# Performance work log

Measured on AMD Instinct MI355X. Metric: run time of the kernel, lower is better.

## Reference

```python
import jax, jax.numpy as jnp
import numpy as np

H, P, G, NS, K = 8, 64, 64, 64, 3          # heads, dim_head, slice_num, d_state, d_conv
D_INNER = H * P                            # 512
CONV_DIM = D_INNER + 2 * NS                # 640
D_IN_PROJ = 2 * D_INNER + 2 * NS + 2 * H   # 1168


def setup_inputs() -> dict:
    key = jax.random.key(0)
    ks = jax.random.split(key, 10)
    dim, Bsz, N = 256, 4, 8192
    s = 0.02
    return {
        "x": jax.random.normal(ks[0], (Bsz, N, dim), jnp.float32),
        "W_fx": jax.random.normal(ks[1], (D_INNER, dim), jnp.float32) * s,
        "b_fx": jnp.zeros((D_INNER,), jnp.float32),
        "W_x": jax.random.normal(ks[2], (D_INNER, dim), jnp.float32) * s,
        "b_x": jnp.zeros((D_INNER,), jnp.float32),
        "W_slice": jax.random.normal(ks[3], (G, P), jnp.float32) * s,
        "b_slice": jnp.zeros((G,), jnp.float32),
        "temperature": jnp.full((1, H, 1, 1), 0.5, jnp.float32),
        "hy_in_w": jax.random.normal(ks[4], (D_IN_PROJ, D_INNER), jnp.float32) * s,
        "hy_conv_w": jax.random.normal(ks[5], (CONV_DIM, K), jnp.float32) * s,
        "hy_conv_b": jnp.zeros((CONV_DIM,), jnp.float32),
        "hy_dt_bias": jnp.log(jnp.expm1(jnp.full((H,), 0.01, jnp.float32))),
        "hy_A_log": jnp.log(jnp.linspace(1.0, 16.0, H)).astype(jnp.float32),
        "hy_D": jnp.ones((H,), jnp.float32),
        "hy_fcD_w": jax.random.normal(ks[6], (H, D_INNER), jnp.float32) * s,
        "hy_norm_w": jnp.ones((D_INNER,), jnp.float32),
        "hy_out_w": jax.random.normal(ks[7], (D_INNER, D_INNER), jnp.float32) * s,
        "out_w": jax.random.normal(ks[8], (dim, D_INNER), jnp.float32) * s,
        "out_b": jnp.zeros((dim,), jnp.float32),
    }


def _hydra(u, in_w, conv_w, conv_b, dt_bias, A_log, Dp, fcD_w, norm_w, out_w):
    # Bidirectional Mamba2-style selective scan (Hydra, non mem-eff path).
    Bt, L, _ = u.shape
    zxbcdt = u @ in_w.T                                   # (B, L, 1168)
    z = zxbcdt[..., :D_INNER]
    xBC = zxbcdt[..., D_INNER:D_INNER + CONV_DIM]
    dt = zxbcdt[..., -2 * H:]
    # fwd dts for fwd copies, time-flipped bwd dts stacked along batch
    dt = jnp.concatenate([dt[..., :H], jnp.flip(dt[..., H:], axis=1)], axis=0)
    dt = jax.nn.softplus(dt + dt_bias)                    # (2B, L, H)
    # depthwise causal conv, kernel K, left pad K-1 then silu
    xp = jnp.pad(xBC, ((0, 0), (K - 1, 0), (0, 0)))
    xBC = sum(xp[:, k:k + L, :] * conv_w[:, k] for k in range(K)) + conv_b
    xBC = jax.nn.silu(xBC)
    x = xBC[..., :D_INNER]
    Bm = xBC[..., D_INNER:D_INNER + NS]
    Cm = xBC[..., D_INNER + NS:]
    x_og = x
    x2 = jnp.concatenate([x, jnp.flip(x, 1)], 0).reshape(2 * Bt, L, H, P)
    B2 = jnp.concatenate([Bm, jnp.flip(Bm, 1)], 0)        # (2B, L, NS)
    C2 = jnp.concatenate([Cm, jnp.flip(Cm, 1)], 0)
    dA = jnp.exp(dt * (-jnp.exp(A_log)))                  # (2B, L, H)
    dBx = jnp.einsum('blh,bln,blhp->blhpn', dt, B2, x2)   # (2B, L, H, P, NS)

    def step(h, inp):
        dA_t, dBx_t, C_t = inp
        h = h * dA_t[:, :, None, None] + dBx_t
        return h, jnp.einsum('bhpn,bn->bhp', h, C_t)

    h0 = jnp.zeros((2 * Bt, H, P, NS), u.dtype)
    _, ys = jax.lax.scan(step, h0, (dA.transpose(1, 0, 2), dBx.transpose(1, 0, 2, 3, 4), C2.transpose(1, 0, 2)))
    y = ys.transpose(1, 0, 2, 3).reshape(2 * Bt, L, D_INNER)
    y_fw, y_bw = y[:Bt], jnp.flip(y[Bt:], 1)
    # quasiseparable: strictly-lower (shift fwd) + strictly-upper (shift bwd) + diagonal
    y = jnp.pad(y_fw[:, :-1], ((0, 0), (1, 0), (0, 0))) + jnp.pad(y_bw[:, 1:], ((0, 0), (0, 1), (0, 0)))
    y = y + x_og * jnp.repeat(x_og @ fcD_w.T + Dp, P, axis=-1)
    # gated RMSNorm (gate before norm), then out projection
    yg = y * jax.nn.silu(z)
    yg = yg * jax.lax.rsqrt(jnp.mean(jnp.square(yg), -1, keepdims=True) + 1e-5) * norm_w
    return yg @ out_w.T


def reference(x, W_fx, b_fx, W_x, b_x, W_slice, b_slice, temperature,
              hy_in_w, hy_conv_w, hy_conv_b, hy_dt_bias, hy_A_log, hy_D,
              hy_fcD_w, hy_norm_w, hy_out_w, out_w, out_b):
    B, N, _ = x.shape
    fx = (x @ W_fx.T + b_fx).reshape(B, N, H, P).transpose(0, 2, 1, 3)   # (B,H,N,P)
    xm = (x @ W_x.T + b_x).reshape(B, N, H, P).transpose(0, 2, 1, 3)
    temp = jnp.maximum(temperature, 1e-6)
    sw = jax.nn.softmax((xm @ W_slice.T + b_slice) / temp, axis=-1)      # (B,H,N,G)
    snorm = sw.sum(2)                                                     # (B,H,G)
    st = jnp.einsum('bhnc,bhng->bhgc', fx, sw) / (snorm + 1e-5)[..., None]
    st = st.transpose(0, 2, 1, 3).reshape(B, G, D_INNER)                  # (B,G,512)
    ot = _hydra(st, hy_in_w, hy_conv_w, hy_conv_b, hy_dt_bias, hy_A_log, hy_D,
                hy_fcD_w, hy_norm_w, hy_out_w)
    ot = ot.reshape(B, G, H, P).transpose(0, 2, 1, 3)                     # (B,H,G,P)
    out = jnp.einsum('bhgc,bhng->bhnc', ot, sw).transpose(0, 2, 1, 3).reshape(B, N, D_INNER)
    return out @ out_w.T + out_b
```

## Files before the change

kernel.cpp:

```cpp
#include <hip/hip_runtime.h>
#include <hip/hip_bf16.h>
#include <cstdint>
#include <cstddef>

#define Hh 8
#define DIN 512
#define CONVD 640
#define DPROJ 1168
#define NTOK 8192
#define DIM 256

typedef __attribute__((ext_vector_type(8))) short short8;
typedef __attribute__((ext_vector_type(4))) float f32x4;

static __device__ __forceinline__ float sigmoidf_(float x) { return 1.f / (1.f + expf(-x)); }
static __device__ __forceinline__ unsigned short f2b(float f) {
  __hip_bfloat16 h = __float2bfloat16(f);
  return *(unsigned short*)&h;
}
static __device__ __forceinline__ float b2f(unsigned short u) {
  union { unsigned int i; float f; } cv; cv.i = ((unsigned int)u) << 16; return cv.f;
}

__global__ __launch_bounds__(256) void k_cvt(
    const float* __restrict__ wfx, const float* __restrict__ wx, const float* __restrict__ outw,
    const float* __restrict__ inw, const float* __restrict__ how,
    const float* __restrict__ bfx, const float* __restrict__ bx,
    unsigned short* __restrict__ wcat, unsigned short* __restrict__ outwb,
    unsigned short* __restrict__ inwb, unsigned short* __restrict__ howb,
    float* __restrict__ bcat) {
  const int e = (blockIdx.x * 256 + threadIdx.x) * 4;
  if (e >= 1253376) {
    const int i = e - 1253376;
    float4 v;
    if (i < 512) v = *(const float4*)(bfx + i);
    else         v = *(const float4*)(bx + (i - 512));
    *(float4*)(bcat + i) = v;
    return;
  }
  const float* src; unsigned short* dst; int i;
  if (e < 131072)        { i = e;           src = wfx;  dst = wcat; }
  else if (e < 262144)   { i = e - 131072;  src = wx;   dst = wcat + 131072; }
  else if (e < 393216)   { i = e - 262144;  src = outw; dst = outwb; }
  else if (e < 991232)   { i = e - 393216;  src = inw;  dst = inwb; }
  else                   { i = e - 991232;  src = how;  dst = howb; }
  float4 v = *(const float4*)(src + i);
  ushort4 o;
  o.x = f2b(v.x); o.y = f2b(v.y); o.z = f2b(v.z); o.w = f2b(v.w);
  *(ushort4*)(dst + i) = o;
}

__global__ __launch_bounds__(256) void k_front(
    const float* __restrict__ x, const unsigned short* __restrict__ wcat,
    const float* __restrict__ bcat, const float* __restrict__ Wslice,
    const float* __restrict__ bslice, const float* __restrict__ temperature,
    unsigned short* __restrict__ cb, unsigned short* __restrict__ swb) {
  __shared__ unsigned short lds[17408];
  unsigned short* As = lds;
  unsigned short* Bs = lds + 8320;
  const int tid = threadIdx.x;
  const int m0 = blockIdx.x * 128;
  const int n0 = blockIdx.y * 128;
  const int w = tid >> 6, lane = tid & 63;
  const int l15 = lane & 15, kq = lane >> 4;
  const int wm = (w & 1) * 64, wn = (w >> 1) * 64;
  float bs[4];
#pragma unroll
  for (int j = 0; j < 4; ++j) bs[j] = bcat[n0 + wn + j * 16 + l15];
  f32x4 acc[4][4];
#pragma unroll
  for (int i = 0; i < 4; ++i)
#pragma unroll
    for (int j = 0; j < 4; ++j) acc[i][j] = (f32x4){0.f, 0.f, 0.f, 0.f};
  for (int kt = 0; kt < 256; kt += 64) {
#pragma unroll
    for (int i = 0; i < 4; ++i) {
      const int c = tid + 256 * i, m = c >> 3, kb = c & 7;
      const float* xs = &x[(size_t)(m0 + m) * 256 + kt + kb * 8];
      float4 v0 = *(const float4*)xs;
      float4 v1 = *(const float4*)(xs + 4);
      short8 av;
      av[0] = (short)f2b(v0.x); av[1] = (short)f2b(v0.y);
      av[2] = (short)f2b(v0.z); av[3] = (short)f2b(v0.w);
      av[4] = (short)f2b(v1.x); av[5] = (short)f2b(v1.y);
      av[6] = (short)f2b(v1.z); av[7] = (short)f2b(v1.w);
      *(short8*)&As[(kb * 130 + m) * 8] = av;
      *(short8*)&Bs[(kb * 130 + m) * 8] = *(const short8*)&wcat[(size_t)(n0 + m) * 256 + kt + kb * 8];
    }
    __syncthreads();
#pragma unroll
    for (int kw = 0; kw < 2; ++kw) {
      short8 af[4], bfr[4];
#pragma unroll
      for (int i = 0; i < 4; ++i) {
        af[i]  = *(const short8*)&As[((kw * 4 + kq) * 130 + wm + i * 16 + l15) * 8];
        bfr[i] = *(const short8*)&Bs[((kw * 4 + kq) * 130 + wn + i * 16 + l15) * 8];
      }
#pragma unroll
      for (int i = 0; i < 4; ++i)
#pragma unroll
        for (int j = 0; j < 4; ++j)
          acc[i][j] = __builtin_amdgcn_mfma_f32_16x16x32_bf16(af[i], bfr[j], acc[i][j], 0, 0, 0);
    }
    __syncthreads();
  }
  unsigned short* Cs = lds;
#pragma unroll
  for (int i = 0; i < 4; ++i)
#pragma unroll
    for (int j = 0; j < 4; ++j)
#pragma unroll
      for (int r = 0; r < 4; ++r) {
        const int m = wm + i * 16 + kq * 4 + r;
        const int n = wn + j * 16 + l15;
        Cs[m * 136 + n] = f2b(acc[i][j][r] + bs[j]);
      }
  __syncthreads();
  if (blockIdx.y < 4) {
#pragma unroll
    for (int it = 0; it < 8; ++it) {
      const int c = tid + 256 * it;
      const int m = c >> 4, seg = c & 15;
      *(short8*)&cb[(size_t)(m0 + m) * 512 + n0 + seg * 8] = *(const short8*)&Cs[m * 136 + seg * 8];
    }
    return;
  }
  const int h0 = (n0 - 512) >> 6;
  const int bidx = m0 >> 13, nb = m0 & (NTOK - 1);
  short8 sbfr[2][4];
#pragma unroll
  for (int kt = 0; kt < 2; ++kt)
#pragma unroll
    for (int j = 0; j < 4; ++j) {
      const float* wp = Wslice + (j * 16 + l15) * 64 + kt * 32 + kq * 8;
      short8 t;
#pragma unroll
      for (int u = 0; u < 8; ++u) t[u] = (short)f2b(wp[u]);
      sbfr[kt][j] = t;
    }
  float sbs[4];
#pragma unroll
  for (int j = 0; j < 4; ++j) sbs[j] = bslice[j * 16 + l15];
  f32x4 sacc[2][2][4];
#pragma unroll
  for (int hl = 0; hl < 2; ++hl)
#pragma unroll
    for (int i = 0; i < 2; ++i)
#pragma unroll
      for (int j = 0; j < 4; ++j) sacc[hl][i][j] = (f32x4){0.f, 0.f, 0.f, 0.f};
#pragma unroll
  for (int hl = 0; hl < 2; ++hl)
#pragma unroll
    for (int kt = 0; kt < 2; ++kt) {
      short8 af[2];
#pragma unroll
      for (int i = 0; i < 2; ++i)
        af[i] = *(const short8*)&Cs[(w * 32 + i * 16 + l15) * 136 + hl * 64 + kt * 32 + kq * 8];
#pragma unroll
      for (int i = 0; i < 2; ++i)
#pragma unroll
        for (int j = 0; j < 4; ++j)
          sacc[hl][i][j] = __builtin_amdgcn_mfma_f32_16x16x32_bf16(af[i], sbfr[kt][j], sacc[hl][i][j], 0, 0, 0);
    }
  __syncthreads();
#pragma unroll
  for (int hl = 0; hl < 2; ++hl) {
    const float invt = 1.f / fmaxf(temperature[h0 + hl], 1e-6f);
#pragma unroll
    for (int i = 0; i < 2; ++i)
#pragma unroll
      for (int r = 0; r < 4; ++r) {
        float v[4];
        float m = -1e30f;
#pragma unroll
        for (int j = 0; j < 4; ++j) { v[j] = (sacc[hl][i][j][r] + sbs[j]) * invt; m = fmaxf(m, v[j]); }
#pragma unroll
        for (int off = 8; off; off >>= 1) m = fmaxf(m, __shfl_xor(m, off));
        float s = 0.f;
#pragma unroll
        for (int j = 0; j < 4; ++j) { v[j] = expf(v[j] - m); s += v[j]; }
#pragma unroll
        for (int off = 8; off; off >>= 1) s += __shfl_xor(s, off);
        const float inv = 1.f / s;
        const int row = w * 32 + i * 16 + kq * 4 + r;
#pragma unroll
        for (int j = 0; j < 4; ++j) Cs[row * 136 + hl * 64 + j * 16 + l15] = f2b(v[j] * inv);
      }
  }
  __syncthreads();
#pragma unroll
  for (int it = 0; it < 8; ++it) {
    const int c = tid + 256 * it;
    const int head = c >> 10, row = (c >> 3) & 127, seg = c & 7;
    *(short8*)&swb[((size_t)(bidx * 8 + h0 + head) * NTOK + nb + row) * 64 + seg * 8] =
        *(const short8*)&Cs[row * 136 + head * 64 + seg * 8];
  }
}

__global__ __launch_bounds__(256) void k_st(
    const unsigned short* __restrict__ swb, const unsigned short* __restrict__ cb,
    float* __restrict__ st_raw, float* __restrict__ snorm) {
  __shared__ unsigned short swT[64][136];
  __shared__ unsigned short fxT[64][136];
  const int tid = threadIdx.x;
  const int bh = blockIdx.y;
  const int b = bh >> 3, h = bh & 7;
  const int nbase = blockIdx.x * 512;
  const int w = tid >> 6, lane = tid & 63;
  const int l15 = lane & 15, kq = lane >> 4;
  f32x4 acc[4];
#pragma unroll
  for (int i = 0; i < 4; ++i) acc[i] = (f32x4){0.f, 0.f, 0.f, 0.f};
  float sn = 0.f;
  for (int nc = 0; nc < 4; ++nc) {
    const int n0 = nbase + nc * 128;
#pragma unroll
    for (int i = 0; i < 4; ++i) {
      const int c = tid + 256 * i, n = c >> 3, gc = c & 7;
      short8 sv = *(const short8*)&swb[((size_t)bh * NTOK + n0 + n) * 64 + gc * 8];
      short8 fv = *(const short8*)&cb[((size_t)(b * NTOK) + n0 + n) * 512 + h * 64 + gc * 8];
#pragma unroll
      for (int u = 0; u < 8; ++u) {
        swT[gc * 8 + u][n] = (unsigned short)sv[u];
        fxT[gc * 8 + u][n] = (unsigned short)fv[u];
      }
    }
    __syncthreads();
    {
      const int g = tid & 63, q = tid >> 6;
#pragma unroll
      for (int nn = 0; nn < 32; ++nn) sn += b2f(swT[g][q * 32 + nn]);
    }
#pragma unroll
    for (int kw = 0; kw < 4; ++kw) {
      short8 bfr = *(const short8*)&fxT[w * 16 + l15][kw * 32 + kq * 8];
#pragma unroll
      for (int mi = 0; mi < 4; ++mi) {
        short8 af = *(const short8*)&swT[mi * 16 + l15][kw * 32 + kq * 8];
        acc[mi] = __builtin_amdgcn_mfma_f32_16x16x32_bf16(af, bfr, acc[mi], 0, 0, 0);
      }
    }
    __syncthreads();
  }
  float* stp = st_raw + (size_t)bh * 4096;
#pragma unroll
  for (int mi = 0; mi < 4; ++mi)
#pragma unroll
    for (int r = 0; r < 4; ++r)
      atomicAdd(&stp[(mi * 16 + kq * 4 + r) * 64 + w * 16 + l15], acc[mi][r]);
  atomicAdd(&snorm[bh * 64 + (tid & 63)], sn);
}

__global__ __launch_bounds__(256) void k_stnorm(
    const float* __restrict__ st_raw, const float* __restrict__ snorm,
    unsigned short* __restrict__ st2b) {
  const int idx = blockIdx.x * 256 + threadIdx.x;
  const int p = idx & 63, g = (idx >> 6) & 63, h = (idx >> 12) & 7, b = idx >> 15;
  const float v = st_raw[idx] / (snorm[(b * Hh + h) * 64 + g] + 1e-5f);
  st2b[(size_t)(b * 64 + g) * DIN + h * 64 + p] = f2b(v);
}

__global__ __launch_bounds__(256) void k_inproj(
    const unsigned short* __restrict__ st2b, const unsigned short* __restrict__ inwb,
    float* __restrict__ zx) {
  const int tid = threadIdx.x;
  const int m0 = blockIdx.x * 64;
  const int n0 = blockIdx.y * 64;
  const int w = tid >> 6, lane = tid & 63;
  const int l15 = lane & 15, kq = lane >> 4;
  f32x4 acc[4];
#pragma unroll
  for (int j = 0; j < 4; ++j) acc[j] = (f32x4){0.f, 0.f, 0.f, 0.f};
  const int arow = m0 + w * 16 + l15;
#pragma unroll
  for (int kc = 0; kc < 16; ++kc) {
    const short8 af = *(const short8*)&st2b[(size_t)arow * DIN + kc * 32 + kq * 8];
#pragma unroll
    for (int j = 0; j < 4; ++j) {
      int brow = n0 + j * 16 + l15;
      if (brow >= DPROJ) brow = 0;
      const short8 bfr = *(const short8*)&inwb[(size_t)brow * DIN + kc * 32 + kq * 8];
      acc[j] = __builtin_amdgcn_mfma_f32_16x16x32_bf16(af, bfr, acc[j], 0, 0, 0);
    }
  }
#pragma unroll
  for (int j = 0; j < 4; ++j)
#pragma unroll
    for (int r = 0; r < 4; ++r) {
      const int m = m0 + w * 16 + kq * 4 + r;
      const int c = n0 + j * 16 + l15;
      if (c < DPROJ) zx[(size_t)m * DPROJ + c] = acc[j][r];
    }
}

__global__ __launch_bounds__(256) void k_prep(
    const float* __restrict__ zx, const float* __restrict__ convw, const float* __restrict__ convb,
    const float* __restrict__ dtbias, const float* __restrict__ Alog,
    float* __restrict__ xbc, float* __restrict__ dt2, float* __restrict__ ldA2) {
  const int idx = blockIdx.x * 256 + threadIdx.x;
  const int NCONV = 4 * 64 * CONVD;
  if (idx < NCONV) {
    const int c = idx % CONVD;
    const int l = (idx / CONVD) & 63;
    const int b = idx / (CONVD * 64);
    float acc = convb[c];
#pragma unroll
    for (int k = 0; k < 3; ++k) {
      const int ls = l - 2 + k;
      if (ls >= 0) acc += zx[(size_t)(b * 64 + ls) * DPROJ + DIN + c] * convw[c * 3 + k];
    }
    xbc[idx] = acc * sigmoidf_(acc);
  } else if (idx < NCONV + 8 * 64 * 8) {
    const int j = idx - NCONV;
    const int h = j & 7, l = (j >> 3) & 63, bb = j >> 9;
    float raw;
    if (bb < 4) raw = zx[(size_t)(bb * 64 + l) * DPROJ + 1152 + h];
    else        raw = zx[(size_t)((bb - 4) * 64 + (63 - l)) * DPROJ + 1160 + h];
    const float d = raw + dtbias[h];
    const float sp = (d > 20.f) ? d : log1pf(expf(d));
    dt2[j] = sp;
    ldA2[j] = sp * -expf(Alog[h]);
  }
}

__global__ __launch_bounds__(256) void k_ssm(
    const float* __restrict__ xbc, const float* __restrict__ dt2, const float* __restrict__ ldA2,
    float* __restrict__ ys) {
  __shared__ unsigned short s_C[64][72];
  __shared__ unsigned short s_Bm[64][72];
  __shared__ unsigned short s_X[64][72];
  __shared__ unsigned short s_G[64][72];
  __shared__ float s_L[64];
  __shared__ float s_dt[64];
  const int blk = blockIdx.x;
  const int h = blk & 7, bb = blk >> 3;
  const int b = (bb < 4) ? bb : bb - 4;
  const bool rev = bb >= 4;
  const int tid = threadIdx.x;
  const int w = tid >> 6, lane = tid & 63;
  const int l15 = lane & 15, kq = lane >> 4;
  {
    const int l = tid >> 2, part = tid & 3;
    const int t = rev ? 63 - l : l;
    const float* src = xbc + (size_t)(b * 64 + l) * CONVD + DIN + part * 32;
#pragma unroll
    for (int u = 0; u < 32; u += 4) {
      float4 v = *(const float4*)(src + u);
      const int c = part * 32 + u;
      unsigned short* dst = (c < 64) ? &s_Bm[t][c] : &s_C[t][c - 64];
      dst[0] = f2b(v.x); dst[1] = f2b(v.y); dst[2] = f2b(v.z); dst[3] = f2b(v.w);
    }
    const float* xs = xbc + (size_t)(b * 64 + l) * CONVD + h * 64 + part * 16;
#pragma unroll
    for (int u = 0; u < 16; u += 4) {
      float4 v = *(const float4*)(xs + u);
      const int p = part * 16 + u;
      s_X[p + 0][t] = f2b(v.x); s_X[p + 1][t] = f2b(v.y);
      s_X[p + 2][t] = f2b(v.z); s_X[p + 3][t] = f2b(v.w);
    }
  }
  if (w == 0) {
    const float dtv = dt2[(bb * 64 + lane) * 8 + h];
    float ld = ldA2[(bb * 64 + lane) * 8 + h];
#pragma unroll
    for (int off = 1; off < 64; off <<= 1) {
      const float o = __shfl_up(ld, off);
      if (lane >= off) ld += o;
    }
    s_L[lane] = ld;
    s_dt[lane] = dtv;
  }
  __syncthreads();
  f32x4 accS[4];
#pragma unroll
  for (int i = 0; i < 4; ++i) accS[i] = (f32x4){0.f, 0.f, 0.f, 0.f};
#pragma unroll
  for (int kw = 0; kw < 2; ++kw) {
    const short8 bfr = *(const short8*)&s_Bm[w * 16 + l15][kw * 32 + kq * 8];
#pragma unroll
    for (int i = 0; i < 4; ++i) {
      const short8 af = *(const short8*)&s_C[i * 16 + l15][kw * 32 + kq * 8];
      accS[i] = __builtin_amdgcn_mfma_f32_16x16x32_bf16(af, bfr, accS[i], 0, 0, 0);
    }
  }
  const int s_idx = w * 16 + l15;
  const float Ls = s_L[s_idx];
  const float dts = s_dt[s_idx];
#pragma unroll
  for (int i = 0; i < 4; ++i)
#pragma unroll
    for (int r = 0; r < 4; ++r) {
      const int t = i * 16 + kq * 4 + r;
      const float g = (s_idx <= t) ? accS[i][r] * expf(s_L[t] - Ls) * dts : 0.f;
      s_G[t][s_idx] = f2b(g);
    }
  __syncthreads();
  f32x4 accY[4];
#pragma unroll
  for (int i = 0; i < 4; ++i) accY[i] = (f32x4){0.f, 0.f, 0.f, 0.f};
#pragma unroll
  for (int kw = 0; kw < 2; ++kw) {
    const short8 bfr = *(const short8*)&s_X[w * 16 + l15][kw * 32 + kq * 8];
#pragma unroll
    for (int i = 0; i < 4; ++i) {
      const short8 af = *(const short8*)&s_G[i * 16 + l15][kw * 32 + kq * 8];
      accY[i] = __builtin_amdgcn_mfma_f32_16x16x32_bf16(af, bfr, accY[i], 0, 0, 0);
    }
  }
#pragma unroll
  for (int i = 0; i < 4; ++i)
#pragma unroll
    for (int r = 0; r < 4; ++r) {
      const int t = i * 16 + kq * 4 + r;
      ys[(((size_t)(bb * 64 + t) * 8 + h) << 6) + w * 16 + l15] = accY[i][r];
    }
}

__global__ __launch_bounds__(256) void k_gate(
    const float* __restrict__ ys, const float* __restrict__ xbc, const float* __restrict__ zx,
    const float* __restrict__ fcdw, const float* __restrict__ Dp,
    const float* __restrict__ normw, unsigned short* __restrict__ ygb) {
  __shared__ float red[256][9];
  __shared__ float s_xfc[8];
  const int bl = blockIdx.x;
  const int b = bl >> 6, l = bl & 63;
  const int tid = threadIdx.x;
  const float xog0 = xbc[(size_t)bl * CONVD + tid];
  const float xog1 = xbc[(size_t)bl * CONVD + 256 + tid];
#pragma unroll
  for (int h = 0; h < 8; ++h)
    red[tid][h] = xog0 * fcdw[h * DIN + tid] + xog1 * fcdw[h * DIN + 256 + tid];
  __syncthreads();
  for (int s = 128; s > 0; s >>= 1) {
    if (tid < s) {
#pragma unroll
      for (int h = 0; h < 8; ++h) red[tid][h] += red[tid + s][h];
    }
    __syncthreads();
  }
  if (tid < 8) s_xfc[tid] = red[0][tid] + Dp[tid];
  __syncthreads();
  float ygv[2];
  float sumsq = 0.f;
#pragma unroll
  for (int ci = 0; ci < 2; ++ci) {
    const int c = tid + ci * 256;
    const int h = c >> 6, p = c & 63;
    float yv = 0.f;
    if (l >= 1)  yv += ys[(((size_t)(b * 64 + (l - 1)) * 8 + h) << 6) + p];
    if (l <= 62) yv += ys[(((size_t)((4 + b) * 64 + (62 - l)) * 8 + h) << 6) + p];
    const float xog = (ci == 0) ? xog0 : xog1;
    yv += xog * s_xfc[h];
    const float z = zx[(size_t)bl * DPROJ + c];
    const float g = yv * (z * sigmoidf_(z));
    ygv[ci] = g;
    sumsq += g * g;
  }
  red[tid][0] = sumsq;
  __syncthreads();
  for (int s = 128; s > 0; s >>= 1) {
    if (tid < s) red[tid][0] += red[tid + s][0];
    __syncthreads();
  }
  const float scale = 1.f / sqrtf(red[0][0] / 512.f + 1e-5f);
#pragma unroll
  for (int ci = 0; ci < 2; ++ci) {
    const int c = tid + ci * 256;
    ygb[(size_t)bl * DIN + c] = f2b(ygv[ci] * scale * normw[c]);
  }
}

__global__ __launch_bounds__(256) void k_oproj(
    const unsigned short* __restrict__ ygb, const unsigned short* __restrict__ howb,
    unsigned short* __restrict__ otT) {
  __shared__ unsigned short Cs[64][72];
  const int tid = threadIdx.x;
  const int b = blockIdx.x;
  const int h = blockIdx.y;
  const int m0 = b * 64, n0 = h * 64;
  const int w = tid >> 6, lane = tid & 63;
  const int l15 = lane & 15, kq = lane >> 4;
  f32x4 acc[4];
#pragma unroll
  for (int j = 0; j < 4; ++j) acc[j] = (f32x4){0.f, 0.f, 0.f, 0.f};
  const int arow = m0 + w * 16 + l15;
#pragma unroll
  for (int kc = 0; kc < 16; ++kc) {
    const short8 af = *(const short8*)&ygb[(size_t)arow * DIN + kc * 32 + kq * 8];
#pragma unroll
    for (int j = 0; j < 4; ++j) {
      const int brow = n0 + j * 16 + l15;
      const short8 bfr = *(const short8*)&howb[(size_t)brow * DIN + kc * 32 + kq * 8];
      acc[j] = __builtin_amdgcn_mfma_f32_16x16x32_bf16(af, bfr, acc[j], 0, 0, 0);
    }
  }
#pragma unroll
  for (int j = 0; j < 4; ++j)
#pragma unroll
    for (int r = 0; r < 4; ++r) {
      const int g = w * 16 + kq * 4 + r;
      const int p = j * 16 + l15;
      Cs[p][g] = f2b(acc[j][r]);
    }
  __syncthreads();
#pragma unroll
  for (int it = 0; it < 2; ++it) {
    const int c = tid + 256 * it;
    const int p = c >> 3, seg = c & 7;
    *(short8*)&otT[(((size_t)(b * 8 + h) * 64 + p) << 6) + seg * 8] = *(const short8*)&Cs[p][seg * 8];
  }
}

__global__ __launch_bounds__(256) void k_mixfinal(
    const unsigned short* __restrict__ swb, const unsigned short* __restrict__ otT,
    const unsigned short* __restrict__ outwb, const float* __restrict__ outb,
    float* __restrict__ out) {
  __shared__ unsigned short lm[33280];
  const int blk = blockIdx.x;
  const int b = blk >> 7;
  const int t0 = (blk & 127) * 64;
  const int tid = threadIdx.x;
  const int w = tid >> 6, lane = tid & 63;
  const int l15 = lane & 15, kq = lane >> 4;
#pragma unroll
  for (int hh = 0; hh < 2; ++hh) {
    const int h = w * 2 + hh;
    const int bh = b * 8 + h;
    f32x4 acc[4][4];
#pragma unroll
    for (int i = 0; i < 4; ++i)
#pragma unroll
      for (int j = 0; j < 4; ++j) acc[i][j] = (f32x4){0.f, 0.f, 0.f, 0.f};
#pragma unroll
    for (int kt = 0; kt < 2; ++kt) {
      short8 af[4], bfr[4];
#pragma unroll
      for (int i = 0; i < 4; ++i) {
        af[i]  = *(const short8*)&swb[((size_t)bh * NTOK + t0 + i * 16 + l15) * 64 + kt * 32 + kq * 8];
        bfr[i] = *(const short8*)&otT[(((size_t)bh * 64 + i * 16 + l15) << 6) + kt * 32 + kq * 8];
      }
#pragma unroll
      for (int i = 0; i < 4; ++i)
#pragma unroll
        for (int j = 0; j < 4; ++j)
          acc[i][j] = __builtin_amdgcn_mfma_f32_16x16x32_bf16(af[i], bfr[j], acc[i][j], 0, 0, 0);
    }
#pragma unroll
    for (int i = 0; i < 4; ++i)
#pragma unroll
      for (int j = 0; j < 4; ++j)
#pragma unroll
        for (int r = 0; r < 4; ++r)
          lm[(i * 16 + kq * 4 + r) * 520 + h * 64 + j * 16 + l15] = f2b(acc[i][j][r]);
  }
  __syncthreads();
  float ob[4];
#pragma unroll
  for (int j = 0; j < 4; ++j) ob[j] = outb[w * 64 + j * 16 + l15];
  f32x4 facc[4][4];
#pragma unroll
  for (int i = 0; i < 4; ++i)
#pragma unroll
    for (int j = 0; j < 4; ++j) facc[i][j] = (f32x4){0.f, 0.f, 0.f, 0.f};
#pragma unroll
  for (int kt = 0; kt < 16; ++kt) {
    short8 af[4], bfr[4];
#pragma unroll
    for (int i = 0; i < 4; ++i) {
      af[i]  = *(const short8*)&lm[(i * 16 + l15) * 520 + kt * 32 + kq * 8];
      bfr[i] = *(const short8*)&outwb[(size_t)(w * 64 + i * 16 + l15) * 512 + kt * 32 + kq * 8];
    }
#pragma unroll
    for (int i = 0; i < 4; ++i)
#pragma unroll
      for (int j = 0; j < 4; ++j)
        facc[i][j] = __builtin_amdgcn_mfma_f32_16x16x32_bf16(af[i], bfr[j], facc[i][j], 0, 0, 0);
  }
  __syncthreads();
  float* lf = (float*)lm;
#pragma unroll
  for (int i = 0; i < 4; ++i)
#pragma unroll
    for (int j = 0; j < 4; ++j)
#pragma unroll
      for (int r = 0; r < 4; ++r)
        lf[(i * 16 + kq * 4 + r) * 260 + w * 64 + j * 16 + l15] = facc[i][j][r] + ob[j];
  __syncthreads();
#pragma unroll
  for (int it = 0; it < 16; ++it) {
    const int c = tid + 256 * it;
    const int row = c >> 6, seg = c & 63;
    *(float4*)&out[((size_t)(b * NTOK + t0 + row)) * 256 + seg * 4] =
        *(const float4*)&lf[row * 260 + seg * 4];
  }
}

extern "C" void kernel_launch(void* const* d_in, const int* in_sizes, int n_in,
                              void* d_out, int out_size, void* d_ws, size_t ws_size,
                              hipStream_t stream) {
  const float* x      = (const float*)d_in[0];
  const float* Wfx    = (const float*)d_in[1];
  const float* bfx    = (const float*)d_in[2];
  const float* Wx     = (const float*)d_in[3];
  const float* bx     = (const float*)d_in[4];
  const float* Wslice = (const float*)d_in[5];
  const float* bslice = (const float*)d_in[6];
  const float* temp   = (const float*)d_in[7];
  const float* inw    = (const float*)d_in[8];
  const float* convw  = (const float*)d_in[9];
  const float* convb  = (const float*)d_in[10];
  const float* dtbias = (const float*)d_in[11];
  const float* Alog   = (const float*)d_in[12];
  const float* Dp     = (const float*)d_in[13];
  const float* fcdw   = (const float*)d_in[14];
  const float* normw  = (const float*)d_in[15];
  const float* how    = (const float*)d_in[16];
  const float* outw   = (const float*)d_in[17];
  const float* outb   = (const float*)d_in[18];

  unsigned short* us = (unsigned short*)d_ws;
  unsigned short* cb     = us;
  unsigned short* swb    = cb + 16777216;
  unsigned short* wcatb  = swb + 16777216;
  unsigned short* outwbf = wcatb + 262144;
  unsigned short* otTb   = outwbf + 131072;
  unsigned short* inwb   = otTb + 131072;
  unsigned short* howb   = inwb + 598016;
  unsigned short* st2b   = howb + 262144;
  unsigned short* ygbb   = st2b + 131072;
  float* fbase = (float*)(ygbb + 131072);
  float* bcat   = fbase;
  float* st_raw = bcat + 1024;
  float* snorm  = st_raw + 131072;
  float* zx     = snorm + 2048;
  float* xbc    = zx + 299008;
  float* dt2    = xbc + 163840;
  float* ldA2   = dt2 + 4096;
  float* ysb    = ldA2 + 4096;

  hipMemsetAsync(st_raw, 0, (131072 + 2048) * sizeof(float), stream);

  k_cvt     <<<dim3(1225),    256, 0, stream>>>(Wfx, Wx, outw, inw, how, bfx, bx,
                                                wcatb, outwbf, inwb, howb, bcat);
  k_front   <<<dim3(256, 8),  256, 0, stream>>>(x, wcatb, bcat, Wslice, bslice, temp, cb, swb);
  k_st      <<<dim3(16, 32),  256, 0, stream>>>(swb, cb, st_raw, snorm);
  k_stnorm  <<<dim3(512),     256, 0, stream>>>(st_raw, snorm, st2b);
  k_inproj  <<<dim3(4, 19),   256, 0, stream>>>(st2b, inwb, zx);
  k_prep    <<<dim3(656),     256, 0, stream>>>(zx, convw, convb, dtbias, Alog, xbc, dt2, ldA2);
  k_ssm     <<<dim3(64),      256, 0, stream>>>(xbc, dt2, ldA2, ysb);
  k_gate    <<<dim3(256),     256, 0, stream>>>(ysb, xbc, zx, fcdw, Dp, normw, ygbb);
  k_oproj   <<<dim3(4, 8),    256, 0, stream>>>(ygbb, howb, otTb);
  k_mixfinal<<<dim3(512),     256, 0, stream>>>(swb, otTb, outwbf, outb, (float*)d_out);
}
```

Measured before the change: 266.9 us.

## Pre-convert x to bf16 and stage front GEMM tiles via global_load_lds

Adds a separate kernel that converts the fp32 input x to bf16 once, so the front GEMM no longer reloads and converts fp32 x in each of its 8 column blocks. The GEMM tile loads now use direct global-to-LDS 16-byte loads, with the LDS layout changed to an unpadded, k-block-major arrangement to suit them. This cuts redundant fp32 x reads and register staging, at the cost of an extra kernel launch, a 16 MB bf16 round trip through memory, and possible LDS bank conflicts now that the padding is gone.

Result: slower. 272.9 us (+2.2%).

```diff
diff --git a/kernel.cpp b/kernel.cpp
--- a/kernel.cpp
+++ b/kernel.cpp
@@ -20,6 +20,10 @@
 }
 static __device__ __forceinline__ float b2f(unsigned short u) {
   union { unsigned int i; float f; } cv; cv.i = ((unsigned int)u) << 16; return cv.f;
+}
+static __device__ __forceinline__ void gll16(const void* g, void* l) {
+  __builtin_amdgcn_global_load_lds((const __attribute__((address_space(1))) void*)g,
+                                   (__attribute__((address_space(3))) void*)l, 16, 0, 0);
 }
 
 __global__ __launch_bounds__(256) void k_cvt(
@@ -50,14 +54,27 @@
   *(ushort4*)(dst + i) = o;
 }
 
+__global__ __launch_bounds__(256) void k_cvtx(
+    const float* __restrict__ x, unsigned short* __restrict__ xb) {
+  const int e = (blockIdx.x * 256 + threadIdx.x) * 8;
+  float4 v0 = *(const float4*)(x + e);
+  float4 v1 = *(const float4*)(x + e + 4);
+  short8 o;
+  o[0] = (short)f2b(v0.x); o[1] = (short)f2b(v0.y);
+  o[2] = (short)f2b(v0.z); o[3] = (short)f2b(v0.w);
+  o[4] = (short)f2b(v1.x); o[5] = (short)f2b(v1.y);
+  o[6] = (short)f2b(v1.z); o[7] = (short)f2b(v1.w);
+  *(short8*)(xb + e) = o;
+}
+
 __global__ __launch_bounds__(256) void k_front(
-    const float* __restrict__ x, const unsigned short* __restrict__ wcat,
+    const unsigned short* __restrict__ xb, const unsigned short* __restrict__ wcat,
     const float* __restrict__ bcat, const float* __restrict__ Wslice,
     const float* __restrict__ bslice, const float* __restrict__ temperature,
     unsigned short* __restrict__ cb, unsigned short* __restrict__ swb) {
   __shared__ unsigned short lds[17408];
   unsigned short* As = lds;
-  unsigned short* Bs = lds + 8320;
+  unsigned short* Bs = lds + 8192;
   const int tid = threadIdx.x;
   const int m0 = blockIdx.x * 128;
   const int n0 = blockIdx.y * 128;
@@ -75,17 +92,10 @@
   for (int kt = 0; kt < 256; kt += 64) {
 #pragma unroll
     for (int i = 0; i < 4; ++i) {
-      const int c = tid + 256 * i, m = c >> 3, kb = c & 7;
-      const float* xs = &x[(size_t)(m0 + m) * 256 + kt + kb * 8];
-      float4 v0 = *(const float4*)xs;
-      float4 v1 = *(const float4*)(xs + 4);
-      short8 av;
-      av[0] = (short)f2b(v0.x); av[1] = (short)f2b(v0.y);
-      av[2] = (short)f2b(v0.z); av[3] = (short)f2b(v0.w);
-      av[4] = (short)f2b(v1.x); av[5] = (short)f2b(v1.y);
-      av[6] = (short)f2b(v1.z); av[7] = (short)f2b(v1.w);
-      *(short8*)&As[(kb * 130 + m) * 8] = av;
-      *(short8*)&Bs[(kb * 130 + m) * 8] = *(const short8*)&wcat[(size_t)(n0 + m) * 256 + kt + kb * 8];
+      const int c = tid + 256 * i;
+      const int kb = c >> 7, m = c & 127;
+      gll16(&xb[(size_t)(m0 + m) * 256 + kt + kb * 8], &As[c * 8]);
+      gll16(&wcat[(size_t)(n0 + m) * 256 + kt + kb * 8], &Bs[c * 8]);
     }
     __syncthreads();
 #pragma unroll
@@ -93,8 +103,8 @@
       short8 af[4], bfr[4];
 #pragma unroll
       for (int i = 0; i < 4; ++i) {
-        af[i]  = *(const short8*)&As[((kw * 4 + kq) * 130 + wm + i * 16 + l15) * 8];
-        bfr[i] = *(const short8*)&Bs[((kw * 4 + kq) * 130 + wn + i * 16 + l15) * 8];
+        af[i]  = *(const short8*)&As[((kw * 4 + kq) * 128 + wm + i * 16 + l15) * 8];
+        bfr[i] = *(const short8*)&Bs[((kw * 4 + kq) * 128 + wn + i * 16 + l15) * 8];
       }
 #pragma unroll
       for (int i = 0; i < 4; ++i)
@@ -628,7 +638,8 @@
   unsigned short* howb   = inwb + 598016;
   unsigned short* st2b   = howb + 262144;
   unsigned short* ygbb   = st2b + 131072;
-  float* fbase = (float*)(ygbb + 131072);
+  unsigned short* xbb    = ygbb + 131072;
+  float* fbase = (float*)(xbb + 8388608);
   float* bcat   = fbase;
   float* st_raw = bcat + 1024;
   float* snorm  = st_raw + 131072;
@@ -642,7 +653,8 @@
 
   k_cvt     <<<dim3(1225),    256, 0, stream>>>(Wfx, Wx, outw, inw, how, bfx, bx,
                                                 wcatb, outwbf, inwb, howb, bcat);
-  k_front   <<<dim3(256, 8),  256, 0, stream>>>(x, wcatb, bcat, Wslice, bslice, temp, cb, swb);
+  k_cvtx    <<<dim3(4096),    256, 0, stream>>>(x, xbb);
+  k_front   <<<dim3(256, 8),  256, 0, stream>>>(xbb, wcatb, bcat, Wslice, bslice, temp, cb, swb);
   k_st      <<<dim3(16, 32),  256, 0, stream>>>(swb, cb, st_raw, snorm);
   k_stnorm  <<<dim3(512),     256, 0, stream>>>(st_raw, snorm, st2b);
   k_inproj  <<<dim3(4, 19),   256, 0, stream>>>(st2b, inwb, zx);
```
